# Optimization experiments

Hardware: AMD Instinct MI355X
Metric: run time of the kernel (lower is better)

The kernel has to match this reference:

```python
import jax, jax.numpy as jnp
import numpy as np

B, S, D = 2, 2048, 1024
H, DH = 16, 64
EPS = 1e-5

def setup_inputs() -> dict:
    key = jax.random.key(0)
    ks = jax.random.split(key, 8)
    s = 0.02
    return {
        "x": jax.random.normal(ks[0], (B, S, D), dtype=jnp.float32),
        "ln_gamma": jnp.ones((D,), jnp.float32),
        "ln_beta": jnp.zeros((D,), jnp.float32),
        "wq": jax.random.normal(ks[1], (D, H * DH), jnp.float32) * s,
        "bq": jnp.zeros((H * DH,), jnp.float32),
        "wk": jax.random.normal(ks[2], (D, H * DH), jnp.float32) * s,
        "bk": jnp.zeros((H * DH,), jnp.float32),
        "wv": jax.random.normal(ks[3], (D, H * DH), jnp.float32) * s,
        "bv": jnp.zeros((H * DH,), jnp.float32),
        "wo": jax.random.normal(ks[4], (H * DH, D), jnp.float32) * s,
        "bo": jnp.zeros((D,), jnp.float32),
    }

def reference(x, ln_gamma, ln_beta, wq, bq, wk, bk, wv, bv, wo, bo):
    # Pre-LayerNorm over d_model
    mu = jnp.mean(x, axis=-1, keepdims=True)
    var = jnp.var(x, axis=-1, keepdims=True)
    xn = (x - mu) * jax.lax.rsqrt(var + EPS) * ln_gamma + ln_beta

    b, s, _ = xn.shape
    q = (xn @ wq + bq).reshape(b, s, H, DH)
    k = (xn @ wk + bk).reshape(b, s, H, DH)
    v = (xn @ wv + bv).reshape(b, s, H, DH)

    scale = jnp.sqrt(jnp.float32(DH))
    scores = jnp.einsum('bihd,bjhd->bhij', q, k) / scale  # [b,h,s,s]
    att = jax.nn.softmax(scores, axis=-1)
    out = jnp.einsum('bhij,bjhd->bihd', att, v).reshape(b, s, H * DH)
    return out @ wo + bo
```

## Files before the change

### kernel.cpp

```cpp
#include <hip/hip_runtime.h>
#include <math.h>

#define SEQ   2048
#define DM    1024
#define NHEAD 16
#define HD    64
#define NTOK  4096
#define EPS   1e-5f
#define SCALE_C 0.18033688f

typedef __attribute__((ext_vector_type(8))) short v8s;
typedef __attribute__((ext_vector_type(4))) short v4s;
typedef __attribute__((ext_vector_type(4))) float v4f;
typedef unsigned short ushort_t;

#define GLOAD16(g, l) __builtin_amdgcn_global_load_lds( \
    (const __attribute__((address_space(1))) unsigned int*)(g), \
    (__attribute__((address_space(3))) unsigned int*)(l), 16, 0, 0)

#if defined(__has_builtin)
#if __has_builtin(__builtin_amdgcn_mfma_f32_16x16x16_bf16)
#define MFMA16(va, vb, vc) __builtin_amdgcn_mfma_f32_16x16x16_bf16(va, vb, vc, 0, 0, 0)
#elif __has_builtin(__builtin_amdgcn_mfma_f32_16x16x16bf16_1k)
#define MFMA16(va, vb, vc) __builtin_amdgcn_mfma_f32_16x16x16bf16_1k(va, vb, vc, 0, 0, 0)
#endif
#endif
#ifndef MFMA16
__device__ __forceinline__ v4f mfma16_asm(v4s a, v4s b, v4f c) {
  asm volatile("s_nop 2\n\tv_mfma_f32_16x16x16_bf16 %0, %1, %2, %0\n\ts_nop 4"
               : "+v"(c) : "v"(a), "v"(b));
  return c;
}
#define MFMA16(va, vb, vc) mfma16_asm(va, vb, vc)
#endif

__device__ __forceinline__ unsigned short f2bf(float f) {
  union { float f; unsigned u; } v; v.f = f;
  unsigned r = v.u + 0x7FFFu + ((v.u >> 16) & 1u);
  return (unsigned short)(r >> 16);
}

__device__ __forceinline__ unsigned pack2_bf16(float a, float b) {
  union { float f; unsigned u; } ua, ub;
  ua.f = a; ub.f = b;
  return __builtin_amdgcn_perm(ub.u + 0x8000u, ua.u + 0x8000u, 0x07060302u);
}

__global__ __launch_bounds__(256) void prep_kernel(
    const float* __restrict__ x, const float* __restrict__ g,
    const float* __restrict__ be, ushort_t* __restrict__ y,
    const float* __restrict__ w0, const float* __restrict__ w1,
    const float* __restrict__ w2, const float* __restrict__ w3,
    ushort_t* __restrict__ o0, ushort_t* __restrict__ o1,
    ushort_t* __restrict__ o2, ushort_t* __restrict__ o3) {
  __shared__ float red[8];
  __shared__ float mu_s, rs_s;
  __shared__ float tile[64][65];
  const int t = threadIdx.x;
  if (blockIdx.x < NTOK) {
    const int row = blockIdx.x;
    const float4 v = ((const float4*)(x + (size_t)row * DM))[t];
    float s  = v.x + v.y + v.z + v.w;
    float ss = v.x*v.x + v.y*v.y + v.z*v.z + v.w*v.w;
    #pragma unroll
    for (int off = 32; off > 0; off >>= 1) {
      s  += __shfl_down(s,  off, 64);
      ss += __shfl_down(ss, off, 64);
    }
    const int wid = t >> 6, lane = t & 63;
    if (lane == 0) { red[wid] = s; red[4 + wid] = ss; }
    __syncthreads();
    if (t == 0) {
      const float S  = red[0] + red[1] + red[2] + red[3];
      const float SS = red[4] + red[5] + red[6] + red[7];
      const float mu  = S * (1.0f / DM);
      const float var = SS * (1.0f / DM) - mu * mu;
      mu_s = mu; rs_s = rsqrtf(var + EPS);
    }
    __syncthreads();
    const float mu = mu_s, r = rs_s;
    const float4 gv = ((const float4*)g)[t];
    const float4 bv = ((const float4*)be)[t];
    ushort4 o;
    o.x = f2bf((v.x - mu) * r * gv.x + bv.x);
    o.y = f2bf((v.y - mu) * r * gv.y + bv.y);
    o.z = f2bf((v.z - mu) * r * gv.z + bv.z);
    o.w = f2bf((v.w - mu) * r * gv.w + bv.w);
    *(ushort4*)(y + (size_t)row * DM + t * 4) = o;
  } else {
    const int i = blockIdx.x - NTOK;
    const int z = i >> 8;
    const float* w = (z==0) ? w0 : (z==1) ? w1 : (z==2) ? w2 : w3;
    ushort_t* o    = (z==0) ? o0 : (z==1) ? o1 : (z==2) ? o2 : o3;
    const int n0 = (i & 15) * 64, k0 = ((i >> 4) & 15) * 64;
    const int r = t >> 4, c4 = (t & 15) * 4;
    #pragma unroll
    for (int ii = 0; ii < 4; ++ii) {
      const float4 v = *(const float4*)(w + (size_t)(k0 + r + ii*16) * DM + n0 + c4);
      tile[r + ii*16][c4 + 0] = v.x;
      tile[r + ii*16][c4 + 1] = v.y;
      tile[r + ii*16][c4 + 2] = v.z;
      tile[r + ii*16][c4 + 3] = v.w;
    }
    __syncthreads();
    #pragma unroll
    for (int ii = 0; ii < 4; ++ii) {
      const int n = r + ii*16;
      ushort4 o4;
      o4.x = f2bf(tile[c4 + 0][n]);
      o4.y = f2bf(tile[c4 + 1][n]);
      o4.z = f2bf(tile[c4 + 2][n]);
      o4.w = f2bf(tile[c4 + 3][n]);
      *(ushort4*)(o + (size_t)(n0 + n) * DM + k0 + c4) = o4;
    }
  }
}

__device__ __forceinline__ void gemm_main(ushort_t* lsa, ushort_t* lsb,
    const ushort_t* A, const ushort_t* WT, int m0, int n0, v4f acc[4][4]) {
  const int tid = threadIdx.x;
  const int wid = tid >> 6, lane = tid & 63;
  const int mh = (wid & 1) << 6, nh = (wid >> 1) << 6;
  const int r16 = lane & 15, quad = lane >> 4;
  const int srow = lane >> 2, sch = lane & 3;
  for (int k0 = 0; k0 < DM; k0 += 64) {
    __syncthreads();
    #pragma unroll
    for (int s = 0; s < 2; ++s) {
      #pragma unroll
      for (int j = 0; j < 2; ++j) {
        const int o = wid * 2 + j;
        GLOAD16(A  + (size_t)(m0 + o*16 + srow) * DM + k0 + s*32 + sch*8, lsa + s*4096 + o*512);
        GLOAD16(WT + (size_t)(n0 + o*16 + srow) * DM + k0 + s*32 + sch*8, lsb + s*4096 + o*512);
      }
    }
    __syncthreads();
    #pragma unroll
    for (int s = 0; s < 2; ++s) {
      v8s af[4], bfr[4];
      #pragma unroll
      for (int i = 0; i < 4; ++i) {
        af[i]  = *(const v8s*)(lsa + s*4096 + (mh + i*16 + r16)*32 + quad*8);
        bfr[i] = *(const v8s*)(lsb + s*4096 + (nh + i*16 + r16)*32 + quad*8);
      }
      #pragma unroll
      for (int i = 0; i < 4; ++i)
        #pragma unroll
        for (int j = 0; j < 4; ++j)
          acc[i][j] = __builtin_amdgcn_mfma_f32_16x16x32_bf16(af[i], bfr[j], acc[i][j], 0, 0, 0);
    }
  }
}

__global__ __launch_bounds__(256, 2) void gemm_qkv(const ushort_t* __restrict__ xn,
    const ushort_t* __restrict__ wtq, const ushort_t* __restrict__ wtk, const ushort_t* __restrict__ wtv,
    const float* __restrict__ bq, const float* __restrict__ bk, const float* __restrict__ bv,
    ushort_t* __restrict__ qo, ushort_t* __restrict__ ko, ushort_t* __restrict__ vto) {
  __shared__ ushort_t lsa[128*64];
  __shared__ ushort_t lsb[128*64];
  const int flat = blockIdx.x;
  const int nf = (flat & 7) * 96 + (flat >> 3);
  const int zi = nf >> 8;
  const int yi = (nf >> 3) & 31;
  const int xi = nf & 7;
  const ushort_t* WT = (zi == 0) ? wtq : (zi == 1) ? wtk : wtv;
  const float* bias  = (zi == 0) ? bq  : (zi == 1) ? bk  : bv;
  const int m0 = yi * 128, n0 = xi * 128;
  v4f acc[4][4];
  #pragma unroll
  for (int i = 0; i < 4; ++i)
    #pragma unroll
    for (int j = 0; j < 4; ++j) acc[i][j] = (v4f){0.f, 0.f, 0.f, 0.f};
  gemm_main(lsa, lsb, xn, WT, m0, n0, acc);
  const int tid = threadIdx.x, wid = tid >> 6, lane = tid & 63;
  const int mh = (wid & 1) << 6, nh = (wid >> 1) << 6;
  const int r16 = lane & 15, quad = lane >> 4;
  if (zi < 2) {
    ushort_t* out = (zi == 0) ? qo : ko;
    const float sc = (zi == 0) ? SCALE_C : 1.0f;
    #pragma unroll
    for (int bn = 0; bn < 4; ++bn) {
      const int col = n0 + nh + bn*16 + r16;
      const float bb = bias[col];
      #pragma unroll
      for (int am = 0; am < 4; ++am) {
        const int tb = m0 + mh + am*16 + quad*4;
        #pragma unroll
        for (int r = 0; r < 4; ++r)
          out[(size_t)(tb + r) * DM + col] = f2bf((acc[am][bn][r] + bb) * sc);
      }
    }
  } else {
    #pragma unroll
    for (int bn = 0; bn < 4; ++bn) {
      const int col = n0 + nh + bn*16 + r16;
      const float bb = bias[col];
      const int h = col >> 6, d = col & 63;
      #pragma unroll
      for (int am = 0; am < 4; ++am) {
        const int tb = m0 + mh + am*16 + quad*4;
        const int b = tb >> 11, t = tb & 2047;
        const int bh = b * NHEAD + h;
        ushort4 o4;
        o4.x = f2bf(acc[am][bn][0] + bb);
        o4.y = f2bf(acc[am][bn][1] + bb);
        o4.z = f2bf(acc[am][bn][2] + bb);
        o4.w = f2bf(acc[am][bn][3] + bb);
        const size_t idx = (size_t)bh * 131072 + (size_t)(t >> 6) * 4096 +
                           (size_t)((((t >> 4) & 3) * 4) + (d >> 4)) * 256 +
                           ((t >> 2) & 3) * 64 + (d & 15) * 4;
        *(ushort4*)(vto + idx) = o4;
      }
    }
  }
}

__global__ __launch_bounds__(256, 2) void gemm_out(const ushort_t* __restrict__ A,
    const ushort_t* __restrict__ WT, const float* __restrict__ bias,
    float* __restrict__ out) {
  __shared__ ushort_t lsa[128*64];
  __shared__ ushort_t lsb[64*64];
  const int flat = blockIdx.x;
  const int nf = (flat & 7) * 64 + (flat >> 3);
  const int n0 = (nf & 15) * 64, m0 = (nf >> 4) * 128;
  const int tid = threadIdx.x;
  const int wid = tid >> 6, lane = tid & 63;
  const int mh = (wid & 1) << 6, nh = (wid >> 1) << 5;
  const int r16 = lane & 15, quad = lane >> 4;
  const int srow = lane >> 2, sch = lane & 3;
  v4f acc[4][2];
  #pragma unroll
  for (int i = 0; i < 4; ++i)
    #pragma unroll
    for (int j = 0; j < 2; ++j) acc[i][j] = (v4f){0.f, 0.f, 0.f, 0.f};
  for (int k0 = 0; k0 < DM; k0 += 64) {
    __syncthreads();
    #pragma unroll
    for (int s = 0; s < 2; ++s) {
      #pragma unroll
      for (int j = 0; j < 2; ++j) {
        const int o = wid * 2 + j;
        GLOAD16(A + (size_t)(m0 + o*16 + srow) * DM + k0 + s*32 + sch*8, lsa + s*4096 + o*512);
      }
      GLOAD16(WT + (size_t)(n0 + wid*16 + srow) * DM + k0 + s*32 + sch*8, lsb + s*2048 + wid*512);
    }
    __syncthreads();
    #pragma unroll
    for (int s = 0; s < 2; ++s) {
      v8s af[4], bfr[2];
      #pragma unroll
      for (int i = 0; i < 4; ++i)
        af[i] = *(const v8s*)(lsa + s*4096 + (mh + i*16 + r16)*32 + quad*8);
      #pragma unroll
      for (int j = 0; j < 2; ++j)
        bfr[j] = *(const v8s*)(lsb + s*2048 + (nh + j*16 + r16)*32 + quad*8);
      #pragma unroll
      for (int i = 0; i < 4; ++i)
        #pragma unroll
        for (int j = 0; j < 2; ++j)
          acc[i][j] = __builtin_amdgcn_mfma_f32_16x16x32_bf16(af[i], bfr[j], acc[i][j], 0, 0, 0);
    }
  }
  #pragma unroll
  for (int bn = 0; bn < 2; ++bn) {
    const int col = n0 + nh + bn*16 + r16;
    const float bb = bias[col];
    #pragma unroll
    for (int am = 0; am < 4; ++am) {
      const int tb = m0 + mh + am*16 + quad*4;
      #pragma unroll
      for (int r = 0; r < 4; ++r)
        out[(size_t)(tb + r) * DM + col] = acc[am][bn][r] + bb;
    }
  }
}

#define OHALF ((size_t)32 * 2048 * 64)
#define LHALF (32 * 2048)
template<int SPLIT>
__global__ __launch_bounds__(256, 4) void attn_kernel(
    const ushort_t* __restrict__ Q, const ushort_t* __restrict__ K,
    const ushort_t* __restrict__ Vt, ushort_t* __restrict__ O,
    float* __restrict__ Opart, float* __restrict__ lpart) {
  __shared__ ushort_t kbuf[8*512];
  __shared__ ushort_t vbuf[8*512];
  const int tid = threadIdx.x, wid = tid >> 6, lane = tid & 63;
  const int r16 = lane & 15, quad = lane >> 4;
  const int q0 = blockIdx.x * 128, bh = blockIdx.y;
  const int half = SPLIT ? blockIdx.z : 0;
  const int b = bh >> 4, h = bh & 15;
  const ushort_t* gQ = Q + (size_t)b * SEQ * DM + h * HD;
  const ushort_t* gK = K + (size_t)b * SEQ * DM + h * HD;
  const ushort_t* gV = Vt + (size_t)bh * 131072;

  const int qt0 = q0 + wid * 32 + r16;
  const int qt1 = qt0 + 16;
  const v8s qf00 = *(const v8s*)(gQ + (size_t)qt0 * DM + quad * 8);
  const v8s qf01 = *(const v8s*)(gQ + (size_t)qt0 * DM + 32 + quad * 8);
  const v8s qf10 = *(const v8s*)(gQ + (size_t)qt1 * DM + quad * 8);
  const v8s qf11 = *(const v8s*)(gQ + (size_t)qt1 * DM + 32 + quad * 8);
  v4f acc0[4], acc1[4];
  #pragma unroll
  for (int i = 0; i < 4; ++i) {
    acc0[i] = (v4f){0.f, 0.f, 0.f, 0.f};
    acc1[i] = (v4f){0.f, 0.f, 0.f, 0.f};
  }
  float lrun0 = 0.f, lrun1 = 0.f;

  const int NIT = SPLIT ? (SEQ / 128) : (SEQ / 64);
  const int kt0 = half * NIT;
  const int o0 = wid * 2, o1 = wid * 2 + 1;
  const ushort_t* srcK0 = gK + (size_t)((o0 >> 1) * 16 + r16) * DM + (o0 & 1) * 32 + quad * 8;
  const ushort_t* srcK1 = gK + (size_t)((o1 >> 1) * 16 + r16) * DM + (o1 & 1) * 32 + quad * 8;
  const ushort_t* srcV  = gV + lane * 8;

  for (int it = 0; it < NIT; ++it) {
    const int kt = kt0 + it;
    const int k0 = kt * 64;
    __syncthreads();
    GLOAD16(srcK0 + (size_t)k0 * DM, kbuf + o0 * 512);
    GLOAD16(srcK1 + (size_t)k0 * DM, kbuf + o1 * 512);
    GLOAD16(srcV + (size_t)kt * 4096 + o0 * 512, vbuf + o0 * 512);
    GLOAD16(srcV + (size_t)kt * 4096 + o1 * 512, vbuf + o1 * 512);
    __syncthreads();

    v4f s0[4], s1[4];
    #pragma unroll
    for (int g = 0; g < 4; ++g) {
      s0[g] = (v4f){0.f, 0.f, 0.f, 0.f};
      s1[g] = (v4f){0.f, 0.f, 0.f, 0.f};
    }
    #pragma unroll
    for (int g = 0; g < 4; ++g) {
      const v8s ka0 = *(const v8s*)(kbuf + (g*2 + 0) * 512 + lane * 8);
      const v8s ka1 = *(const v8s*)(kbuf + (g*2 + 1) * 512 + lane * 8);
      s0[g] = __builtin_amdgcn_mfma_f32_16x16x32_bf16(ka0, qf00, s0[g], 0, 0, 0);
      s0[g] = __builtin_amdgcn_mfma_f32_16x16x32_bf16(ka1, qf01, s0[g], 0, 0, 0);
      s1[g] = __builtin_amdgcn_mfma_f32_16x16x32_bf16(ka0, qf10, s1[g], 0, 0, 0);
      s1[g] = __builtin_amdgcn_mfma_f32_16x16x32_bf16(ka1, qf11, s1[g], 0, 0, 0);
    }

    v4s pf0[4], pf1[4];
    float ls0 = 0.f, ls1 = 0.f;
    #pragma unroll
    for (int g = 0; g < 4; ++g) {
      float e0 = __builtin_amdgcn_exp2f(s0[g][0]);
      float e1 = __builtin_amdgcn_exp2f(s0[g][1]);
      float e2 = __builtin_amdgcn_exp2f(s0[g][2]);
      float e3 = __builtin_amdgcn_exp2f(s0[g][3]);
      ls0 += (e0 + e1) + (e2 + e3);
      union { v4s s; uint2 u; } pk;
      pk.u.x = pack2_bf16(e0, e1);
      pk.u.y = pack2_bf16(e2, e3);
      pf0[g] = pk.s;
      float f0 = __builtin_amdgcn_exp2f(s1[g][0]);
      float f1 = __builtin_amdgcn_exp2f(s1[g][1]);
      float f2 = __builtin_amdgcn_exp2f(s1[g][2]);
      float f3 = __builtin_amdgcn_exp2f(s1[g][3]);
      ls1 += (f0 + f1) + (f2 + f3);
      union { v4s s; uint2 u; } pk2;
      pk2.u.x = pack2_bf16(f0, f1);
      pk2.u.y = pack2_bf16(f2, f3);
      pf1[g] = pk2.s;
    }
    ls0 += __shfl_xor(ls0, 16, 64);
    ls0 += __shfl_xor(ls0, 32, 64);
    lrun0 += ls0;
    ls1 += __shfl_xor(ls1, 16, 64);
    ls1 += __shfl_xor(ls1, 32, 64);
    lrun1 += ls1;

    #pragma unroll
    for (int dg = 0; dg < 4; ++dg) {
      #pragma unroll
      for (int g = 0; g < 4; ++g) {
        const v4s vf = *(const v4s*)(vbuf + (g*4 + dg) * 256 + quad * 64 + r16 * 4);
        acc0[dg] = MFMA16(vf, pf0[g], acc0[dg]);
        acc1[dg] = MFMA16(vf, pf1[g], acc1[dg]);
      }
    }
  }

  if (SPLIT) {
    float* Op0 = Opart + half * OHALF + ((size_t)bh * SEQ + qt0) * 64;
    float* Op1 = Opart + half * OHALF + ((size_t)bh * SEQ + qt1) * 64;
    #pragma unroll
    for (int dg = 0; dg < 4; ++dg) {
      *(v4f*)(Op0 + dg*16 + quad*4) = acc0[dg];
      *(v4f*)(Op1 + dg*16 + quad*4) = acc1[dg];
    }
    if (quad == 0) {
      lpart[half * LHALF + bh * SEQ + qt0] = lrun0;
      lpart[half * LHALF + bh * SEQ + qt1] = lrun1;
    }
  } else {
    const float inv0 = 1.f / lrun0, inv1 = 1.f / lrun1;
    ushort_t* gO = O + (size_t)b * SEQ * DM + h * HD;
    #pragma unroll
    for (int dg = 0; dg < 4; ++dg) {
      ushort4 o4;
      o4.x = f2bf(acc0[dg][0] * inv0);
      o4.y = f2bf(acc0[dg][1] * inv0);
      o4.z = f2bf(acc0[dg][2] * inv0);
      o4.w = f2bf(acc0[dg][3] * inv0);
      *(ushort4*)(gO + (size_t)qt0 * DM + dg*16 + quad*4) = o4;
      ushort4 o5;
      o5.x = f2bf(acc1[dg][0] * inv1);
      o5.y = f2bf(acc1[dg][1] * inv1);
      o5.z = f2bf(acc1[dg][2] * inv1);
      o5.w = f2bf(acc1[dg][3] * inv1);
      *(ushort4*)(gO + (size_t)qt1 * DM + dg*16 + quad*4) = o5;
    }
  }
}

__global__ __launch_bounds__(256) void combine_kernel(
    const float* __restrict__ Opart, const float* __restrict__ lpart,
    ushort_t* __restrict__ ob) {
  const int tok = blockIdx.x;
  const int b = tok >> 11, t = tok & 2047;
  const int dm0 = threadIdx.x * 4;
  const int h = dm0 >> 6, d = dm0 & 63;
  const int bh = b * NHEAD + h;
  const size_t idx = ((size_t)bh * SEQ + t) * 64 + d;
  const float4 a = *(const float4*)(Opart + idx);
  const float4 c = *(const float4*)(Opart + OHALF + idx);
  const float l = lpart[bh * SEQ + t] + lpart[LHALF + bh * SEQ + t];
  const float inv = 1.f / l;
  ushort4 o4;
  o4.x = f2bf((a.x + c.x) * inv);
  o4.y = f2bf((a.y + c.y) * inv);
  o4.z = f2bf((a.z + c.z) * inv);
  o4.w = f2bf((a.w + c.w) * inv);
  *(ushort4*)(ob + (size_t)tok * DM + dm0) = o4;
}

extern "C" void kernel_launch(void* const* d_in, const int* in_sizes, int n_in,
                              void* d_out, int out_size, void* d_ws, size_t ws_size,
                              hipStream_t stream) {
  const float* x     = (const float*)d_in[0];
  const float* gamma = (const float*)d_in[1];
  const float* beta  = (const float*)d_in[2];
  const float* wq    = (const float*)d_in[3];
  const float* bq    = (const float*)d_in[4];
  const float* wk    = (const float*)d_in[5];
  const float* bk    = (const float*)d_in[6];
  const float* wv    = (const float*)d_in[7];
  const float* bv    = (const float*)d_in[8];
  const float* wo    = (const float*)d_in[9];
  const float* bo    = (const float*)d_in[10];
  float* out = (float*)d_out;

  unsigned char* w8 = (unsigned char*)d_ws;
  const size_t MB = 1024 * 1024;
  ushort_t* xn  = (ushort_t*)(w8 + 0 * MB);
  ushort_t* qb  = (ushort_t*)(w8 + 8 * MB);
  ushort_t* kb  = (ushort_t*)(w8 + 16 * MB);
  ushort_t* vt  = (ushort_t*)(w8 + 24 * MB);
  ushort_t* wtq = (ushort_t*)(w8 + 32 * MB);
  ushort_t* wtk = (ushort_t*)(w8 + 34 * MB);
  ushort_t* wtv = (ushort_t*)(w8 + 36 * MB);
  ushort_t* wto = (ushort_t*)(w8 + 38 * MB);
  float* Opart  = (float*)(w8 + 40 * MB);
  float* lpart  = (float*)(w8 + 72 * MB);
  ushort_t* ob  = xn;

  prep_kernel<<<dim3(NTOK + 1024), dim3(256), 0, stream>>>(
      x, gamma, beta, xn, wq, wk, wv, wo, wtq, wtk, wtv, wto);
  gemm_qkv<<<dim3(768), dim3(256), 0, stream>>>(xn, wtq, wtk, wtv, bq, bk, bv, qb, kb, vt);
  if (ws_size >= 73 * MB) {
    attn_kernel<1><<<dim3(SEQ / 128, 2 * NHEAD, 2), dim3(256), 0, stream>>>(
        qb, kb, vt, nullptr, Opart, lpart);
    combine_kernel<<<dim3(NTOK), dim3(256), 0, stream>>>(Opart, lpart, ob);
  } else {
    attn_kernel<0><<<dim3(SEQ / 128, 2 * NHEAD, 1), dim3(256), 0, stream>>>(
        qb, kb, vt, ob, nullptr, nullptr);
  }
  gemm_out<<<dim3(512), dim3(256), 0, stream>>>(ob, wto, bo, out);
}
```

Measured before the change: 199.1 us.

## Merge split-KV attention halves into one 512-thread block with LDS combine

Replaces the two-block split of the key range plus a separate combine kernel with one 512-thread block. Two 4-wave groups each process half the keys and reduce their partial outputs and row sums through shared memory. This drops the fp32 partial-output global writes and reads and one kernel launch. In exchange each block is larger, shares one barrier across both halves, and uses more LDS, which may lower occupancy.

```diff
diff --git a/kernel.cpp b/kernel.cpp
--- a/kernel.cpp
+++ b/kernel.cpp
@@ -275,25 +275,24 @@
   }
 }
 
-#define OHALF ((size_t)32 * 2048 * 64)
-#define LHALF (32 * 2048)
-template<int SPLIT>
-__global__ __launch_bounds__(256, 4) void attn_kernel(
+__global__ __launch_bounds__(512, 4) void attn_kernel(
     const ushort_t* __restrict__ Q, const ushort_t* __restrict__ K,
-    const ushort_t* __restrict__ Vt, ushort_t* __restrict__ O,
-    float* __restrict__ Opart, float* __restrict__ lpart) {
-  __shared__ ushort_t kbuf[8*512];
-  __shared__ ushort_t vbuf[8*512];
+    const ushort_t* __restrict__ Vt, ushort_t* __restrict__ O) {
+  __shared__ ushort_t smem[16384];
+  __shared__ float lred[128];
   const int tid = threadIdx.x, wid = tid >> 6, lane = tid & 63;
   const int r16 = lane & 15, quad = lane >> 4;
+  const int w4 = wid & 3, half = wid >> 2;
   const int q0 = blockIdx.x * 128, bh = blockIdx.y;
-  const int half = SPLIT ? blockIdx.z : 0;
   const int b = bh >> 4, h = bh & 15;
   const ushort_t* gQ = Q + (size_t)b * SEQ * DM + h * HD;
   const ushort_t* gK = K + (size_t)b * SEQ * DM + h * HD;
   const ushort_t* gV = Vt + (size_t)bh * 131072;
 
-  const int qt0 = q0 + wid * 32 + r16;
+  ushort_t* kb = smem + half * 4096;
+  ushort_t* vb = smem + 8192 + half * 4096;
+
+  const int qt0 = q0 + w4 * 32 + r16;
   const int qt1 = qt0 + 16;
   const v8s qf00 = *(const v8s*)(gQ + (size_t)qt0 * DM + quad * 8);
   const v8s qf01 = *(const v8s*)(gQ + (size_t)qt0 * DM + 32 + quad * 8);
@@ -307,9 +306,9 @@
   }
   float lrun0 = 0.f, lrun1 = 0.f;
 
-  const int NIT = SPLIT ? (SEQ / 128) : (SEQ / 64);
+  const int NIT = SEQ / 128;
   const int kt0 = half * NIT;
-  const int o0 = wid * 2, o1 = wid * 2 + 1;
+  const int o0 = w4 * 2, o1 = o0 + 1;
   const ushort_t* srcK0 = gK + (size_t)((o0 >> 1) * 16 + r16) * DM + (o0 & 1) * 32 + quad * 8;
   const ushort_t* srcK1 = gK + (size_t)((o1 >> 1) * 16 + r16) * DM + (o1 & 1) * 32 + quad * 8;
   const ushort_t* srcV  = gV + lane * 8;
@@ -318,10 +317,10 @@
     const int kt = kt0 + it;
     const int k0 = kt * 64;
     __syncthreads();
-    GLOAD16(srcK0 + (size_t)k0 * DM, kbuf + o0 * 512);
-    GLOAD16(srcK1 + (size_t)k0 * DM, kbuf + o1 * 512);
-    GLOAD16(srcV + (size_t)kt * 4096 + o0 * 512, vbuf + o0 * 512);
-    GLOAD16(srcV + (size_t)kt * 4096 + o1 * 512, vbuf + o1 * 512);
+    GLOAD16(srcK0 + (size_t)k0 * DM, kb + o0 * 512);
+    GLOAD16(srcK1 + (size_t)k0 * DM, kb + o1 * 512);
+    GLOAD16(srcV + (size_t)kt * 4096 + o0 * 512, vb + o0 * 512);
+    GLOAD16(srcV + (size_t)kt * 4096 + o1 * 512, vb + o1 * 512);
     __syncthreads();
 
     v4f s0[4], s1[4];
@@ -332,8 +331,8 @@
     }
     #pragma unroll
     for (int g = 0; g < 4; ++g) {
-      const v8s ka0 = *(const v8s*)(kbuf + (g*2 + 0) * 512 + lane * 8);
-      const v8s ka1 = *(const v8s*)(kbuf + (g*2 + 1) * 512 + lane * 8);
+      const v8s ka0 = *(const v8s*)(kb + (g*2 + 0) * 512 + lane * 8);
+      const v8s ka1 = *(const v8s*)(kb + (g*2 + 1) * 512 + lane * 8);
       s0[g] = __builtin_amdgcn_mfma_f32_16x16x32_bf16(ka0, qf00, s0[g], 0, 0, 0);
       s0[g] = __builtin_amdgcn_mfma_f32_16x16x32_bf16(ka1, qf01, s0[g], 0, 0, 0);
       s1[g] = __builtin_amdgcn_mfma_f32_16x16x32_bf16(ka0, qf10, s1[g], 0, 0, 0);
@@ -374,65 +373,47 @@
     for (int dg = 0; dg < 4; ++dg) {
       #pragma unroll
       for (int g = 0; g < 4; ++g) {
-        const v4s vf = *(const v4s*)(vbuf + (g*4 + dg) * 256 + quad * 64 + r16 * 4);
+        const v4s vf = *(const v4s*)(vb + (g*4 + dg) * 256 + quad * 64 + r16 * 4);
         acc0[dg] = MFMA16(vf, pf0[g], acc0[dg]);
         acc1[dg] = MFMA16(vf, pf1[g], acc1[dg]);
       }
     }
   }
 
-  if (SPLIT) {
-    float* Op0 = Opart + half * OHALF + ((size_t)bh * SEQ + qt0) * 64;
-    float* Op1 = Opart + half * OHALF + ((size_t)bh * SEQ + qt1) * 64;
+  __syncthreads();
+  float* facc = (float*)smem;
+  const int row0 = w4 * 32 + r16, row1 = row0 + 16;
+  if (half == 1) {
     #pragma unroll
     for (int dg = 0; dg < 4; ++dg) {
-      *(v4f*)(Op0 + dg*16 + quad*4) = acc0[dg];
-      *(v4f*)(Op1 + dg*16 + quad*4) = acc1[dg];
-    }
-    if (quad == 0) {
-      lpart[half * LHALF + bh * SEQ + qt0] = lrun0;
-      lpart[half * LHALF + bh * SEQ + qt1] = lrun1;
-    }
-  } else {
-    const float inv0 = 1.f / lrun0, inv1 = 1.f / lrun1;
+      *(v4f*)(facc + row0 * 64 + dg * 16 + quad * 4) = acc0[dg];
+      *(v4f*)(facc + row1 * 64 + dg * 16 + quad * 4) = acc1[dg];
+    }
+    if (quad == 0) { lred[row0] = lrun0; lred[row1] = lrun1; }
+  }
+  __syncthreads();
+  if (half == 0) {
+    const float inv0 = 1.f / (lrun0 + lred[row0]);
+    const float inv1 = 1.f / (lrun1 + lred[row1]);
     ushort_t* gO = O + (size_t)b * SEQ * DM + h * HD;
     #pragma unroll
     for (int dg = 0; dg < 4; ++dg) {
+      const v4f u0 = acc0[dg] + *(const v4f*)(facc + row0 * 64 + dg * 16 + quad * 4);
+      const v4f u1 = acc1[dg] + *(const v4f*)(facc + row1 * 64 + dg * 16 + quad * 4);
       ushort4 o4;
-      o4.x = f2bf(acc0[dg][0] * inv0);
-      o4.y = f2bf(acc0[dg][1] * inv0);
-      o4.z = f2bf(acc0[dg][2] * inv0);
-      o4.w = f2bf(acc0[dg][3] * inv0);
+      o4.x = f2bf(u0[0] * inv0);
+      o4.y = f2bf(u0[1] * inv0);
+      o4.z = f2bf(u0[2] * inv0);
+      o4.w = f2bf(u0[3] * inv0);
       *(ushort4*)(gO + (size_t)qt0 * DM + dg*16 + quad*4) = o4;
       ushort4 o5;
-      o5.x = f2bf(acc1[dg][0] * inv1);
-      o5.y = f2bf(acc1[dg][1] * inv1);
-      o5.z = f2bf(acc1[dg][2] * inv1);
-      o5.w = f2bf(acc1[dg][3] * inv1);
+      o5.x = f2bf(u1[0] * inv1);
+      o5.y = f2bf(u1[1] * inv1);
+      o5.z = f2bf(u1[2] * inv1);
+      o5.w = f2bf(u1[3] * inv1);
       *(ushort4*)(gO + (size_t)qt1 * DM + dg*16 + quad*4) = o5;
     }
   }
-}
-
-__global__ __launch_bounds__(256) void combine_kernel(
-    const float* __restrict__ Opart, const float* __restrict__ lpart,
-    ushort_t* __restrict__ ob) {
-  const int tok = blockIdx.x;
-  const int b = tok >> 11, t = tok & 2047;
-  const int dm0 = threadIdx.x * 4;
-  const int h = dm0 >> 6, d = dm0 & 63;
-  const int bh = b * NHEAD + h;
-  const size_t idx = ((size_t)bh * SEQ + t) * 64 + d;
-  const float4 a = *(const float4*)(Opart + idx);
-  const float4 c = *(const float4*)(Opart + OHALF + idx);
-  const float l = lpart[bh * SEQ + t] + lpart[LHALF + bh * SEQ + t];
-  const float inv = 1.f / l;
-  ushort4 o4;
-  o4.x = f2bf((a.x + c.x) * inv);
-  o4.y = f2bf((a.y + c.y) * inv);
-  o4.z = f2bf((a.z + c.z) * inv);
-  o4.w = f2bf((a.w + c.w) * inv);
-  *(ushort4*)(ob + (size_t)tok * DM + dm0) = o4;
 }
 
 extern "C" void kernel_launch(void* const* d_in, const int* in_sizes, int n_in,
@@ -461,20 +442,11 @@
   ushort_t* wtk = (ushort_t*)(w8 + 34 * MB);
   ushort_t* wtv = (ushort_t*)(w8 + 36 * MB);
   ushort_t* wto = (ushort_t*)(w8 + 38 * MB);
-  float* Opart  = (float*)(w8 + 40 * MB);
-  float* lpart  = (float*)(w8 + 72 * MB);
   ushort_t* ob  = xn;
 
   prep_kernel<<<dim3(NTOK + 1024), dim3(256), 0, stream>>>(
       x, gamma, beta, xn, wq, wk, wv, wo, wtq, wtk, wtv, wto);
   gemm_qkv<<<dim3(768), dim3(256), 0, stream>>>(xn, wtq, wtk, wtv, bq, bk, bv, qb, kb, vt);
-  if (ws_size >= 73 * MB) {
-    attn_kernel<1><<<dim3(SEQ / 128, 2 * NHEAD, 2), dim3(256), 0, stream>>>(
-        qb, kb, vt, nullptr, Opart, lpart);
-    combine_kernel<<<dim3(NTOK), dim3(256), 0, stream>>>(Opart, lpart, ob);
-  } else {
-    attn_kernel<0><<<dim3(SEQ / 128, 2 * NHEAD, 1), dim3(256), 0, stream>>>(
-        qb, kb, vt, ob, nullptr, nullptr);
-  }
+  attn_kernel<<<dim3(SEQ / 128, 2 * NHEAD), dim3(512), 0, stream>>>(qb, kb, vt, ob);
   gemm_out<<<dim3(512), dim3(256), 0, stream>>>(ob, wto, bo, out);
 }
```

New measurement: 191.8 us. 1.04x faster.
